# Optimization experiments

Hardware: AMD Instinct MI355X
Metric: run time of the kernel (lower is better)

## Reference

```python
import jax, jax.numpy as jnp
import numpy as np

N_PP = 8192      # number of papers (nodes_num_pp)
N_A = 8192       # number of authors
N_AP = N_PP + N_A  # nodes_num_ap (stacked paper+author id space)
DIM = 16
E = 262144
ALPHA = 0.5


def _cdist(x, y):
    # Euclidean cdist via Gram trick; avoids (B, A, D) broadcast intermediate.
    x2 = jnp.sum(x * x, axis=-1)[:, None]
    y2 = jnp.sum(y * y, axis=-1)[None, :]
    d2 = x2 + y2 - 2.0 * (x @ y.T)
    return jnp.sqrt(jnp.maximum(d2, 0.0))


def setup_inputs() -> dict:
    key = jax.random.key(0)
    ks = jax.random.split(key, 8)
    p_star = jax.random.normal(ks[0], (N_PP, DIM), dtype=jnp.float32)
    p = jax.random.normal(ks[1], (N_PP, DIM), dtype=jnp.float32)
    a = jax.random.normal(ks[2], (N_A, DIM), dtype=jnp.float32)
    beta_ap = 2.0 * jax.random.uniform(ks[3], (N_AP,), dtype=jnp.float32) - 1.0
    gamma_pp = 2.0 * jax.random.uniform(ks[4], (2 * N_PP,), dtype=jnp.float32) - 1.0
    edges_pp = jax.random.randint(ks[5], (2, E), 0, N_PP)
    e_ap0 = jax.random.randint(ks[6], (E,), 0, N_PP)
    e_ap1 = jax.random.randint(ks[7], (E,), N_PP, N_AP)
    edges_ap = jnp.stack([e_ap0, e_ap1])
    p_star_nodes = jnp.arange(N_PP, dtype=jnp.int32)
    p_nodes = jnp.arange(N_PP, dtype=jnp.int32)
    a_nodes = jnp.arange(N_A, dtype=jnp.int32) + N_PP
    return {"p_star": p_star, "p": p, "a": a, "beta_ap": beta_ap,
            "gamma_pp": gamma_pp, "edges_pp": edges_pp, "edges_ap": edges_ap,
            "p_star_nodes": p_star_nodes, "p_nodes": p_nodes, "a_nodes": a_nodes}


def reference(p_star, p, a, beta_ap, gamma_pp, edges_pp, edges_ap,
              p_star_nodes, p_nodes, a_nodes):
    # ---------- paper-paper (pp) term ----------
    ps_sel = p_star[p_star_nodes]                    # (B, D)
    p_sel = p[p_nodes]                               # (P, D)
    g_ps = gamma_pp[p_star_nodes]                    # (B,)
    g_p = gamma_pp[p_nodes + N_PP]                   # (P,)
    # gamma_mat.T - dist_mat, shape (B, P)
    m_pp = jnp.exp(g_ps[:, None] + g_p[None, :] - _cdist(ps_sel, p_sel))
    nonlink_pp = jnp.sum(jnp.triu(m_pp, k=1))        # strict upper triangle
    gamma_pair = gamma_pp[edges_pp[0]] + gamma_pp[edges_pp[1] + N_PP]
    d_pp = jnp.linalg.norm(p_star[edges_pp[0]] - p[edges_pp[1]], axis=-1)
    link_pp = jnp.sum(gamma_pair - d_pp)
    nll_pp = -(link_pp - nonlink_pp)

    # ---------- author-paper (ap) term ----------
    a_sel = a[a_nodes - N_PP]                        # (A, D)
    b_ps = beta_ap[p_star_nodes]                     # (B,)
    b_a = beta_ap[a_nodes]                           # (A,)
    # intended math: beta_mat.T - dist_mat, shape (B, A)
    m_ap = jnp.exp(b_ps[:, None] + b_a[None, :] - _cdist(ps_sel, a_sel))
    nonlink_ap = jnp.sum(m_ap)
    beta_pair = beta_ap[edges_ap[0]] + beta_ap[edges_ap[1]]
    d_ap = jnp.linalg.norm(p_star[edges_ap[0]] - a[edges_ap[1] - N_PP], axis=-1)
    link_ap = jnp.sum(beta_pair - d_ap)
    nll_ap = -(link_ap - nonlink_ap)

    n_p = p_nodes.shape[0]
    n_a = a_nodes.shape[0]
    return ALPHA * nll_pp / n_p + (1.0 - ALPHA) * nll_ap / n_a
```

## Files before the change

kernel.cpp:

```cpp
#include <hip/hip_runtime.h>
#include <stdint.h>

#define N_PP   8192
#define N_A    8192
#define DIM    16
#define NEDGE  262144
#define LOG2E  1.4426950408889634f
#define CH     32

#define WS_PSBF 64
#define WS_PBF  (WS_PSBF + 65536)
#define WS_ABF  (WS_PBF  + 65536)
#define WS_X2PS (WS_ABF  + 65536)
#define WS_Y2P  (WS_X2PS + 8192)
#define WS_Y2A  (WS_Y2P  + 8192)
#define WS_EGC  (WS_Y2A  + 8192)
#define WS_EBC  (WS_EGC  + 8192)
#define WS_GL2  (WS_EBC  + 8192)
#define WS_BL2  (WS_GL2  + 8192)

#define NB_AP  512
#define NB_PP  512
#define NB_EPP 256
#define NB_EAP 256
#define NB_TOTAL (NB_AP + NB_PP + NB_EPP + NB_EAP)

typedef short    bf16x8 __attribute__((ext_vector_type(8)));
typedef float    f32x4  __attribute__((ext_vector_type(4)));
typedef unsigned u32x4  __attribute__((ext_vector_type(4)));

__device__ __forceinline__ float waveReduce(float v) {
#pragma unroll
    for (int off = 32; off > 0; off >>= 1)
        v += __shfl_down(v, off, 64);
    return v;
}

__device__ __forceinline__ unsigned bf16_rne(float f) {
    unsigned u = __builtin_bit_cast(unsigned, f);
    return (u + 0x7FFFu + ((u >> 16) & 1u)) >> 16;
}
__device__ __forceinline__ unsigned packbf2(float a, float b) {
    return bf16_rne(a) | (bf16_rne(b) << 16);
}

__device__ __forceinline__ void gload_lds(const uint32_t* g, uint32_t* l) {
    __builtin_amdgcn_global_load_lds(
        (const __attribute__((address_space(1))) void*)(uintptr_t)g,
        (__attribute__((address_space(3))) void*)(unsigned)(uintptr_t)l,
        16, 0, 0);
}

__global__ __launch_bounds__(256) void precompute_kernel(
    const float* __restrict__ p_star, const float* __restrict__ p,
    const float* __restrict__ a, const float* __restrict__ beta_ap,
    const float* __restrict__ gamma_pp, float* __restrict__ ws)
{
    const int g = blockIdx.x * 256 + threadIdx.x;
    if (g < 8) ws[g] = 0.0f;

    if (g < 3 * 8192) {
        const int arr = g >> 13, idx = g & 8191;
        const float* src = arr == 0 ? p_star : (arr == 1 ? p : a);
        const int bfo = arr == 0 ? WS_PSBF : (arr == 1 ? WS_PBF : WS_ABF);
        const int n2o = arr == 0 ? WS_X2PS : (arr == 1 ? WS_Y2P : WS_Y2A);
        const float4* rp = (const float4*)(src + idx * DIM);
        float4 f0 = rp[0], f1 = rp[1], f2 = rp[2], f3 = rp[3];
        float n2 = f0.x*f0.x + f0.y*f0.y + f0.z*f0.z + f0.w*f0.w
                 + f1.x*f1.x + f1.y*f1.y + f1.z*f1.z + f1.w*f1.w
                 + f2.x*f2.x + f2.y*f2.y + f2.z*f2.z + f2.w*f2.w
                 + f3.x*f3.x + f3.y*f3.y + f3.z*f3.z + f3.w*f3.w;
        u32x4 u0 = { packbf2(f0.x, f0.y), packbf2(f0.z, f0.w),
                     packbf2(f1.x, f1.y), packbf2(f1.z, f1.w) };
        u32x4 u1 = { packbf2(f2.x, f2.y), packbf2(f2.z, f2.w),
                     packbf2(f3.x, f3.y), packbf2(f3.z, f3.w) };
        u32x4* dst = (u32x4*)(ws + bfo) + idx * 2;
        dst[0] = u0; dst[1] = u1;
        ws[n2o + idx] = n2;
    } else if (g < 7 * 8192) {
        const int h = g - 3 * 8192, q = h >> 13, i = h & 8191;
        if      (q == 0) ws[WS_EGC + i] = __expf(gamma_pp[8192 + i]);
        else if (q == 1) ws[WS_EBC + i] = __expf(beta_ap[8192 + i]);
        else if (q == 2) ws[WS_GL2 + i] = gamma_pp[i] * LOG2E;
        else             ws[WS_BL2 + i] = beta_ap[i] * LOG2E;
    }
}

__global__ void main_kernel(
    const float* __restrict__ p_star, const float* __restrict__ p,
    const float* __restrict__ a, const float* __restrict__ beta_ap,
    const float* __restrict__ gamma_pp, const int* __restrict__ edges_pp,
    const int* __restrict__ edges_ap, float* __restrict__ ws,
    float* __restrict__ out)
{
    __shared__ uint32_t sbuf[5120];
    __shared__ float smred[4];
    const int b = blockIdx.x, tid = threadIdx.x, wid = tid >> 6;
    const int lane = tid & 63, quad = lane >> 4, l16 = lane & 15;

    float val = 0.f;
    int slot;

    if (b < NB_AP + NB_PP) {
        const bool isPP = (b >= NB_AP);
        const int  bb   = isPP ? b - NB_AP : b;
        const int  g    = isPP ? 127 - (bb >> 2) : (bb >> 2);
        const int  q    = bb & 3;
        const int  s    = (g << 2) + wid;
        slot = isPP ? 0 : 2;

        const uint32_t* Xbf = (const uint32_t*)(ws + WS_PSBF);
        const uint32_t* Ybf = (const uint32_t*)(ws + (isPP ? WS_PBF : WS_ABF));
        const float* x2a = ws + WS_X2PS;
        const float* y2  = ws + (isPP ? WS_Y2P : WS_Y2A);
        const float* gl2 = ws + (isPP ? WS_GL2 : WS_BL2);
        const float* EcA = ws + (isPP ? WS_EGC : WS_EBC);

        const int j = (s << 4) + l16;
        u32x4 bu = {0u, 0u, 0u, 0u};
        if (quad < 2) bu = *(const u32x4*)(Ybf + j * 8 + (quad << 2));
        const bf16x8 bfrag = __builtin_bit_cast(bf16x8, bu);
        const float y2c = y2[j];
        const float Ec  = EcA[j];
        const f32x4 zero4 = {0.f, 0.f, 0.f, 0.f};

        const int len = isPP ? ((g << 2) + 4) : 512;
        const int nch = (len + CH - 1) / CH;
        const int c0 = (q * nch) >> 2, c1 = ((q + 1) * nch) >> 2;

        float acc = 0.f;
        for (int c = c0; c < c1; ++c) {
            const int t0 = c << 5;
            __syncthreads();
            for (int k = wid; k < 20; k += 4) {
                const uint32_t* gsrc;
                int loff;
                if (k < 16)      { gsrc = Xbf + (t0 << 7) + (k << 8);
                                   loff = k << 8; }
                else if (k < 18) { gsrc = (const uint32_t*)(x2a + (t0 << 4)) + ((k - 16) << 8);
                                   loff = 4096 + ((k - 16) << 8); }
                else             { gsrc = (const uint32_t*)(gl2 + (t0 << 4)) + ((k - 18) << 8);
                                   loff = 4608 + ((k - 18) << 8); }
                gload_lds(gsrc + (lane << 2), &sbuf[loff]);
            }
            __syncthreads();
            const int tF = isPP ? (s < t0 + CH ? s : t0 + CH) : t0 + CH;
            for (int t = t0; t < tF; ++t) {
                const int tl = t - t0;
                u32x4 au = {0u, 0u, 0u, 0u};
                if (quad < 2)
                    au = *(const u32x4*)&sbuf[(tl << 7) + (l16 << 3) + (quad << 2)];
                const f32x4 x24 = *(const f32x4*)((const float*)sbuf + 4096 + (tl << 4) + (quad << 2));
                const f32x4 ag4 = *(const f32x4*)((const float*)sbuf + 4608 + (tl << 4) + (quad << 2));
                f32x4 d = __builtin_amdgcn_mfma_f32_16x16x32_bf16(
                    __builtin_bit_cast(bf16x8, au), bfrag, zero4, 0, 0, 0);
#pragma unroll
                for (int r = 0; r < 4; ++r) {
                    float d2 = fmaf(-2.f, d[r], x24[r] + y2c);
                    d2 = fmaxf(d2, 0.f);
                    acc += __builtin_amdgcn_exp2f(
                        fmaf(-LOG2E, __builtin_amdgcn_sqrtf(d2), ag4[r]));
                }
            }
            if (isPP && s >= t0 && s < t0 + CH) {
                const int tl = s - t0;
                u32x4 au = {0u, 0u, 0u, 0u};
                if (quad < 2)
                    au = *(const u32x4*)&sbuf[(tl << 7) + (l16 << 3) + (quad << 2)];
                const f32x4 x24 = *(const f32x4*)((const float*)sbuf + 4096 + (tl << 4) + (quad << 2));
                const f32x4 ag4 = *(const f32x4*)((const float*)sbuf + 4608 + (tl << 4) + (quad << 2));
                f32x4 d = __builtin_amdgcn_mfma_f32_16x16x32_bf16(
                    __builtin_bit_cast(bf16x8, au), bfrag, zero4, 0, 0, 0);
#pragma unroll
                for (int r = 0; r < 4; ++r) {
                    float d2 = fmaf(-2.f, d[r], x24[r] + y2c);
                    d2 = fmaxf(d2, 0.f);
                    float term = __builtin_amdgcn_exp2f(
                        fmaf(-LOG2E, __builtin_amdgcn_sqrtf(d2), ag4[r]));
                    if (l16 <= (quad << 2) + r) term = 0.f;
                    acc += term;
                }
            }
        }
        val = acc * Ec;
    } else {
        const int  eb   = b - (NB_AP + NB_PP);
        const bool isPP = (eb < NB_EPP);
        const int  base = (isPP ? eb : eb - NB_EPP) * 256 + tid;
        slot = isPP ? 1 : 3;
        float sum = 0.f;
#pragma unroll
        for (int k = 0; k < 4; ++k) {
            const int e = base + k * 65536;
            const float* yrow;
            float bias;
            int e0;
            if (isPP) {
                e0 = edges_pp[e];
                int e1 = edges_pp[NEDGE + e];
                yrow = p + e1 * DIM;
                bias = gamma_pp[e0] + gamma_pp[N_PP + e1];
            } else {
                e0 = edges_ap[e];
                int e1 = edges_ap[NEDGE + e];
                yrow = a + (e1 - N_PP) * DIM;
                bias = beta_ap[e0] + beta_ap[e1];
            }
            const float4* xp = (const float4*)(p_star + e0 * DIM);
            const float4* yp = (const float4*)yrow;
            float d2 = 0.f;
#pragma unroll
            for (int kk = 0; kk < 4; ++kk) {
                float4 xv = xp[kk], yv = yp[kk];
                float dx = xv.x - yv.x, dy = xv.y - yv.y,
                      dz = xv.z - yv.z, dw = xv.w - yv.w;
                d2 += dx*dx + dy*dy + dz*dz + dw*dw;
            }
            sum += bias - __builtin_amdgcn_sqrtf(d2);
        }
        val = sum;
    }

    float wsum = waveReduce(val);
    if ((tid & 63) == 0) smred[wid] = wsum;
    __syncthreads();
    if (tid == 0) {
        atomicAdd(&ws[slot], smred[0] + smred[1] + smred[2] + smred[3]);
        __threadfence();
        unsigned old = atomicAdd((unsigned*)(ws + 4), 1u);
        if (old == NB_TOTAL - 1) {
            float s0 = atomicAdd(&ws[0], 0.f), s1 = atomicAdd(&ws[1], 0.f);
            float s2 = atomicAdd(&ws[2], 0.f), s3 = atomicAdd(&ws[3], 0.f);
            out[0] = 0.5f * (s0 - s1) / (float)N_PP
                   + 0.5f * (s2 - s3) / (float)N_A;
        }
    }
}

extern "C" void kernel_launch(void* const* d_in, const int* in_sizes, int n_in,
                              void* d_out, int out_size, void* d_ws, size_t ws_size,
                              hipStream_t stream) {
    const float* p_star   = (const float*)d_in[0];
    const float* p        = (const float*)d_in[1];
    const float* a        = (const float*)d_in[2];
    const float* beta_ap  = (const float*)d_in[3];
    const float* gamma_pp = (const float*)d_in[4];
    const int*   edges_pp = (const int*)d_in[5];
    const int*   edges_ap = (const int*)d_in[6];

    float* ws  = (float*)d_ws;
    float* out = (float*)d_out;

    hipLaunchKernelGGL(precompute_kernel, dim3(224), dim3(256), 0, stream,
                       p_star, p, a, beta_ap, gamma_pp, ws);
    hipLaunchKernelGGL(main_kernel, dim3(NB_TOTAL), dim3(256), 0, stream,
                       p_star, p, a, beta_ap, gamma_pp, edges_pp, edges_ap, ws, out);
}
```

Before: 146.0 us.

## Move edge sums into precompute kernel and retile pairwise blocks per chunk

```diff
diff --git a/kernel.cpp b/kernel.cpp
--- a/kernel.cpp
+++ b/kernel.cpp
@@ -2,28 +2,25 @@
 #include <stdint.h>
 
 #define N_PP   8192
-#define N_A    8192
 #define DIM    16
 #define NEDGE  262144
 #define LOG2E  1.4426950408889634f
-#define CH     32
-
-#define WS_PSBF 64
-#define WS_PBF  (WS_PSBF + 65536)
-#define WS_ABF  (WS_PBF  + 65536)
-#define WS_X2PS (WS_ABF  + 65536)
-#define WS_Y2P  (WS_X2PS + 8192)
-#define WS_Y2A  (WS_Y2P  + 8192)
-#define WS_EGC  (WS_Y2A  + 8192)
-#define WS_EBC  (WS_EGC  + 8192)
-#define WS_GL2  (WS_EBC  + 8192)
-#define WS_BL2  (WS_GL2  + 8192)
-
-#define NB_AP  512
-#define NB_PP  512
-#define NB_EPP 256
-#define NB_EAP 256
-#define NB_TOTAL (NB_AP + NB_PP + NB_EPP + NB_EAP)
+
+#define WS_EDGE  8
+#define WS_PSBF  512
+#define WS_PBF   (WS_PSBF + 65536)
+#define WS_ABF   (WS_PBF  + 65536)
+#define WS_X2PS  (WS_ABF  + 65536)
+#define WS_Y2P   (WS_X2PS + 8192)
+#define WS_Y2A   (WS_Y2P  + 8192)
+#define WS_EGC   (WS_Y2A  + 8192)
+#define WS_EBC   (WS_EGC  + 8192)
+#define WS_GL2   (WS_EBC  + 8192)
+#define WS_BL2   (WS_GL2  + 8192)
+
+#define NQ_AP  1024
+#define NQ_PP  544
+#define NB_MAT (NQ_AP + NQ_PP)
 
 typedef short    bf16x8 __attribute__((ext_vector_type(8)));
 typedef float    f32x4  __attribute__((ext_vector_type(4)));
@@ -51,147 +48,51 @@
         16, 0, 0);
 }
 
-__global__ __launch_bounds__(256) void precompute_kernel(
-    const float* __restrict__ p_star, const float* __restrict__ p,
-    const float* __restrict__ a, const float* __restrict__ beta_ap,
-    const float* __restrict__ gamma_pp, float* __restrict__ ws)
-{
-    const int g = blockIdx.x * 256 + threadIdx.x;
-    if (g < 8) ws[g] = 0.0f;
-
-    if (g < 3 * 8192) {
-        const int arr = g >> 13, idx = g & 8191;
-        const float* src = arr == 0 ? p_star : (arr == 1 ? p : a);
-        const int bfo = arr == 0 ? WS_PSBF : (arr == 1 ? WS_PBF : WS_ABF);
-        const int n2o = arr == 0 ? WS_X2PS : (arr == 1 ? WS_Y2P : WS_Y2A);
-        const float4* rp = (const float4*)(src + idx * DIM);
-        float4 f0 = rp[0], f1 = rp[1], f2 = rp[2], f3 = rp[3];
-        float n2 = f0.x*f0.x + f0.y*f0.y + f0.z*f0.z + f0.w*f0.w
-                 + f1.x*f1.x + f1.y*f1.y + f1.z*f1.z + f1.w*f1.w
-                 + f2.x*f2.x + f2.y*f2.y + f2.z*f2.z + f2.w*f2.w
-                 + f3.x*f3.x + f3.y*f3.y + f3.z*f3.z + f3.w*f3.w;
-        u32x4 u0 = { packbf2(f0.x, f0.y), packbf2(f0.z, f0.w),
-                     packbf2(f1.x, f1.y), packbf2(f1.z, f1.w) };
-        u32x4 u1 = { packbf2(f2.x, f2.y), packbf2(f2.z, f2.w),
-                     packbf2(f3.x, f3.y), packbf2(f3.z, f3.w) };
-        u32x4* dst = (u32x4*)(ws + bfo) + idx * 2;
-        dst[0] = u0; dst[1] = u1;
-        ws[n2o + idx] = n2;
-    } else if (g < 7 * 8192) {
-        const int h = g - 3 * 8192, q = h >> 13, i = h & 8191;
-        if      (q == 0) ws[WS_EGC + i] = __expf(gamma_pp[8192 + i]);
-        else if (q == 1) ws[WS_EBC + i] = __expf(beta_ap[8192 + i]);
-        else if (q == 2) ws[WS_GL2 + i] = gamma_pp[i] * LOG2E;
-        else             ws[WS_BL2 + i] = beta_ap[i] * LOG2E;
-    }
-}
-
-__global__ void main_kernel(
+__global__ __launch_bounds__(256) void pre_kernel(
     const float* __restrict__ p_star, const float* __restrict__ p,
     const float* __restrict__ a, const float* __restrict__ beta_ap,
     const float* __restrict__ gamma_pp, const int* __restrict__ edges_pp,
-    const int* __restrict__ edges_ap, float* __restrict__ ws,
-    float* __restrict__ out)
+    const int* __restrict__ edges_ap, float* __restrict__ ws)
 {
-    __shared__ uint32_t sbuf[5120];
-    __shared__ float smred[4];
-    const int b = blockIdx.x, tid = threadIdx.x, wid = tid >> 6;
-    const int lane = tid & 63, quad = lane >> 4, l16 = lane & 15;
-
-    float val = 0.f;
-    int slot;
-
-    if (b < NB_AP + NB_PP) {
-        const bool isPP = (b >= NB_AP);
-        const int  bb   = isPP ? b - NB_AP : b;
-        const int  g    = isPP ? 127 - (bb >> 2) : (bb >> 2);
-        const int  q    = bb & 3;
-        const int  s    = (g << 2) + wid;
-        slot = isPP ? 0 : 2;
-
-        const uint32_t* Xbf = (const uint32_t*)(ws + WS_PSBF);
-        const uint32_t* Ybf = (const uint32_t*)(ws + (isPP ? WS_PBF : WS_ABF));
-        const float* x2a = ws + WS_X2PS;
-        const float* y2  = ws + (isPP ? WS_Y2P : WS_Y2A);
-        const float* gl2 = ws + (isPP ? WS_GL2 : WS_BL2);
-        const float* EcA = ws + (isPP ? WS_EGC : WS_EBC);
-
-        const int j = (s << 4) + l16;
-        u32x4 bu = {0u, 0u, 0u, 0u};
-        if (quad < 2) bu = *(const u32x4*)(Ybf + j * 8 + (quad << 2));
-        const bf16x8 bfrag = __builtin_bit_cast(bf16x8, bu);
-        const float y2c = y2[j];
-        const float Ec  = EcA[j];
-        const f32x4 zero4 = {0.f, 0.f, 0.f, 0.f};
-
-        const int len = isPP ? ((g << 2) + 4) : 512;
-        const int nch = (len + CH - 1) / CH;
-        const int c0 = (q * nch) >> 2, c1 = ((q + 1) * nch) >> 2;
-
-        float acc = 0.f;
-        for (int c = c0; c < c1; ++c) {
-            const int t0 = c << 5;
-            __syncthreads();
-            for (int k = wid; k < 20; k += 4) {
-                const uint32_t* gsrc;
-                int loff;
-                if (k < 16)      { gsrc = Xbf + (t0 << 7) + (k << 8);
-                                   loff = k << 8; }
-                else if (k < 18) { gsrc = (const uint32_t*)(x2a + (t0 << 4)) + ((k - 16) << 8);
-                                   loff = 4096 + ((k - 16) << 8); }
-                else             { gsrc = (const uint32_t*)(gl2 + (t0 << 4)) + ((k - 18) << 8);
-                                   loff = 4608 + ((k - 18) << 8); }
-                gload_lds(gsrc + (lane << 2), &sbuf[loff]);
-            }
-            __syncthreads();
-            const int tF = isPP ? (s < t0 + CH ? s : t0 + CH) : t0 + CH;
-            for (int t = t0; t < tF; ++t) {
-                const int tl = t - t0;
-                u32x4 au = {0u, 0u, 0u, 0u};
-                if (quad < 2)
-                    au = *(const u32x4*)&sbuf[(tl << 7) + (l16 << 3) + (quad << 2)];
-                const f32x4 x24 = *(const f32x4*)((const float*)sbuf + 4096 + (tl << 4) + (quad << 2));
-                const f32x4 ag4 = *(const f32x4*)((const float*)sbuf + 4608 + (tl << 4) + (quad << 2));
-                f32x4 d = __builtin_amdgcn_mfma_f32_16x16x32_bf16(
-                    __builtin_bit_cast(bf16x8, au), bfrag, zero4, 0, 0, 0);
-#pragma unroll
-                for (int r = 0; r < 4; ++r) {
-                    float d2 = fmaf(-2.f, d[r], x24[r] + y2c);
-                    d2 = fmaxf(d2, 0.f);
-                    acc += __builtin_amdgcn_exp2f(
-                        fmaf(-LOG2E, __builtin_amdgcn_sqrtf(d2), ag4[r]));
-                }
-            }
-            if (isPP && s >= t0 && s < t0 + CH) {
-                const int tl = s - t0;
-                u32x4 au = {0u, 0u, 0u, 0u};
-                if (quad < 2)
-                    au = *(const u32x4*)&sbuf[(tl << 7) + (l16 << 3) + (quad << 2)];
-                const f32x4 x24 = *(const f32x4*)((const float*)sbuf + 4096 + (tl << 4) + (quad << 2));
-                const f32x4 ag4 = *(const f32x4*)((const float*)sbuf + 4608 + (tl << 4) + (quad << 2));
-                f32x4 d = __builtin_amdgcn_mfma_f32_16x16x32_bf16(
-                    __builtin_bit_cast(bf16x8, au), bfrag, zero4, 0, 0, 0);
-#pragma unroll
-                for (int r = 0; r < 4; ++r) {
-                    float d2 = fmaf(-2.f, d[r], x24[r] + y2c);
-                    d2 = fmaxf(d2, 0.f);
-                    float term = __builtin_amdgcn_exp2f(
-                        fmaf(-LOG2E, __builtin_amdgcn_sqrtf(d2), ag4[r]));
-                    if (l16 <= (quad << 2) + r) term = 0.f;
-                    acc += term;
-                }
-            }
-        }
-        val = acc * Ec;
+    const int b = blockIdx.x, tid = threadIdx.x;
+
+    if (b < 224) {
+        const int g = b * 256 + tid;
+        if (g < 8) ws[g] = 0.0f;
+        if (g < 3 * 8192) {
+            const int arr = g >> 13, idx = g & 8191;
+            const float* src = arr == 0 ? p_star : (arr == 1 ? p : a);
+            const int bfo = arr == 0 ? WS_PSBF : (arr == 1 ? WS_PBF : WS_ABF);
+            const int n2o = arr == 0 ? WS_X2PS : (arr == 1 ? WS_Y2P : WS_Y2A);
+            const float4* rp = (const float4*)(src + idx * DIM);
+            float4 f0 = rp[0], f1 = rp[1], f2 = rp[2], f3 = rp[3];
+            float n2 = f0.x*f0.x + f0.y*f0.y + f0.z*f0.z + f0.w*f0.w
+                     + f1.x*f1.x + f1.y*f1.y + f1.z*f1.z + f1.w*f1.w
+                     + f2.x*f2.x + f2.y*f2.y + f2.z*f2.z + f2.w*f2.w
+                     + f3.x*f3.x + f3.y*f3.y + f3.z*f3.z + f3.w*f3.w;
+            u32x4 u0 = { packbf2(f0.x, f0.y), packbf2(f0.z, f0.w),
+                         packbf2(f1.x, f1.y), packbf2(f1.z, f1.w) };
+            u32x4 u1 = { packbf2(f2.x, f2.y), packbf2(f2.z, f2.w),
+                         packbf2(f3.x, f3.y), packbf2(f3.z, f3.w) };
+            u32x4* dst = (u32x4*)(ws + bfo) + idx * 2;
+            dst[0] = u0; dst[1] = u1;
+            ws[n2o + idx] = n2;
+        } else if (g < 7 * 8192) {
+            const int h = g - 3 * 8192, q = h >> 13, i = h & 8191;
+            if      (q == 0) ws[WS_EGC + i] = __expf(gamma_pp[8192 + i]);
+            else if (q == 1) ws[WS_EBC + i] = __expf(beta_ap[8192 + i]);
+            else if (q == 2) ws[WS_GL2 + i] = gamma_pp[i] * LOG2E;
+            else             ws[WS_BL2 + i] = beta_ap[i] * LOG2E;
+        }
     } else {
-        const int  eb   = b - (NB_AP + NB_PP);
-        const bool isPP = (eb < NB_EPP);
-        const int  base = (isPP ? eb : eb - NB_EPP) * 256 + tid;
-        slot = isPP ? 1 : 3;
+        __shared__ float smred[4];
+        const int  eb   = b - 224;
+        const bool isPP = (eb < 128);
+        const int  base = (isPP ? eb : eb - 128) * 2048;
         float sum = 0.f;
 #pragma unroll
-        for (int k = 0; k < 4; ++k) {
-            const int e = base + k * 65536;
+        for (int k = 0; k < 8; ++k) {
+            const int e = base + k * 256 + tid;
             const float* yrow;
             float bias;
             int e0;
@@ -218,21 +119,122 @@
             }
             sum += bias - __builtin_amdgcn_sqrtf(d2);
         }
-        val = sum;
-    }
+        float wsum = waveReduce(sum);
+        if ((tid & 63) == 0) smred[tid >> 6] = wsum;
+        __syncthreads();
+        if (tid == 0)
+            ws[WS_EDGE + eb] = smred[0] + smred[1] + smred[2] + smred[3];
+    }
+}
+
+__global__ void main_kernel(float* __restrict__ ws, float* __restrict__ out)
+{
+    __shared__ uint32_t sbuf[5120];
+    __shared__ float smred[4];
+    const int b = blockIdx.x, tid = threadIdx.x, wid = tid >> 6;
+    const int lane = tid & 63, quad = lane >> 4, l16 = lane & 15;
+
+    const bool isPP = (b >= NQ_AP);
+    int g, c;
+    if (!isPP) { g = b >> 4; c = b & 15; }
+    else {
+        const int qq = b - NQ_AP;
+        int bnd = 0;
+        while (2 * (bnd + 1) * (bnd + 2) <= qq) ++bnd;
+        const int r = qq - 2 * bnd * (bnd + 1);
+        g = 4 * bnd + r / (bnd + 1);
+        c = r % (bnd + 1);
+    }
+    const int t0 = c << 5;
+
+    const uint32_t* Xbf = (const uint32_t*)(ws + WS_PSBF);
+    const uint32_t* Ybf = (const uint32_t*)(ws + (isPP ? WS_PBF : WS_ABF));
+    const float* x2a = ws + WS_X2PS;
+    const float* y2  = ws + (isPP ? WS_Y2P : WS_Y2A);
+    const float* gl2 = ws + (isPP ? WS_GL2 : WS_BL2);
+    const float* EcA = ws + (isPP ? WS_EGC : WS_EBC);
+
+    const int sA = (g << 3) + (wid << 1);
+    bf16x8 bfrag[2];
+    float  y2c[2], Ec[2];
+#pragma unroll
+    for (int ss = 0; ss < 2; ++ss) {
+        const int j = ((sA + ss) << 4) + l16;
+        u32x4 bu = {0u, 0u, 0u, 0u};
+        if (quad < 2) bu = *(const u32x4*)(Ybf + j * 8 + (quad << 2));
+        bfrag[ss] = __builtin_bit_cast(bf16x8, bu);
+        y2c[ss] = y2[j];
+        Ec[ss]  = EcA[j];
+    }
+
+    for (int k = wid; k < 20; k += 4) {
+        const uint32_t* gsrc;
+        int loff;
+        if (k < 16)      { gsrc = Xbf + (t0 << 7) + (k << 8);            loff = k << 8; }
+        else if (k < 18) { gsrc = (const uint32_t*)(x2a + (t0 << 4)) + ((k - 16) << 8);
+                           loff = 4096 + ((k - 16) << 8); }
+        else             { gsrc = (const uint32_t*)(gl2 + (t0 << 4)) + ((k - 18) << 8);
+                           loff = 4608 + ((k - 18) << 8); }
+        gload_lds(gsrc + (lane << 2), &sbuf[loff]);
+    }
+    __syncthreads();
+
+    const f32x4 zero4 = {0.f, 0.f, 0.f, 0.f};
+    float acc[2] = {0.f, 0.f};
+    const int tHi = isPP ? (sA + 1 < t0 + 32 ? sA + 2 : t0 + 32) : t0 + 32;
+    for (int t = t0; t < tHi; ++t) {
+        const int tl = t - t0;
+        const u32x4 au = *(const u32x4*)&sbuf[(tl << 7) + (l16 << 3) + ((quad & 1) << 2)];
+        const f32x4 x24 = *(const f32x4*)((const float*)sbuf + 4096 + (tl << 4) + (quad << 2));
+        const f32x4 ag4 = *(const f32x4*)((const float*)sbuf + 4608 + (tl << 4) + (quad << 2));
+#pragma unroll
+        for (int ss = 0; ss < 2; ++ss) {
+            const int s = sA + ss;
+            if (isPP && t > s) continue;
+            f32x4 d = __builtin_amdgcn_mfma_f32_16x16x32_bf16(
+                __builtin_bit_cast(bf16x8, au), bfrag[ss], zero4, 0, 0, 0);
+            if (!isPP || t < s) {
+#pragma unroll
+                for (int r = 0; r < 4; ++r) {
+                    float d2 = fmaf(-2.f, d[r], x24[r] + y2c[ss]);
+                    d2 = fmaxf(d2, 0.f);
+                    acc[ss] += __builtin_amdgcn_exp2f(
+                        fmaf(-LOG2E, __builtin_amdgcn_sqrtf(d2), ag4[r]));
+                }
+            } else {
+#pragma unroll
+                for (int r = 0; r < 4; ++r) {
+                    float d2 = fmaf(-2.f, d[r], x24[r] + y2c[ss]);
+                    d2 = fmaxf(d2, 0.f);
+                    float term = __builtin_amdgcn_exp2f(
+                        fmaf(-LOG2E, __builtin_amdgcn_sqrtf(d2), ag4[r]));
+                    if (l16 <= (quad << 2) + r) term = 0.f;
+                    acc[ss] += term;
+                }
+            }
+        }
+    }
+    const float val = acc[0] * Ec[0] + acc[1] * Ec[1];
 
     float wsum = waveReduce(val);
     if ((tid & 63) == 0) smred[wid] = wsum;
     __syncthreads();
     if (tid == 0) {
-        atomicAdd(&ws[slot], smred[0] + smred[1] + smred[2] + smred[3]);
+        atomicAdd(&ws[isPP ? 2 : 0], smred[0] + smred[1] + smred[2] + smred[3]);
         __threadfence();
         unsigned old = atomicAdd((unsigned*)(ws + 4), 1u);
-        if (old == NB_TOTAL - 1) {
-            float s0 = atomicAdd(&ws[0], 0.f), s1 = atomicAdd(&ws[1], 0.f);
-            float s2 = atomicAdd(&ws[2], 0.f), s3 = atomicAdd(&ws[3], 0.f);
-            out[0] = 0.5f * (s0 - s1) / (float)N_PP
-                   + 0.5f * (s2 - s3) / (float)N_A;
+        if (old == NB_MAT - 1) {
+            float s0 = atomicAdd(&ws[0], 0.f);
+            float s2 = atomicAdd(&ws[2], 0.f);
+            float lpp = 0.f, lap = 0.f;
+            for (int i = 0; i < 128; i += 4) {
+                const float4 v = *(const float4*)(ws + WS_EDGE + i);
+                const float4 u = *(const float4*)(ws + WS_EDGE + 128 + i);
+                lpp += v.x + v.y + v.z + v.w;
+                lap += u.x + u.y + u.z + u.w;
+            }
+            out[0] = 0.5f * (s0 - lpp) / (float)N_PP
+                   + 0.5f * (s2 - lap) / (float)N_PP;
         }
     }
 }
@@ -251,8 +253,7 @@
     float* ws  = (float*)d_ws;
     float* out = (float*)d_out;
 
-    hipLaunchKernelGGL(precompute_kernel, dim3(224), dim3(256), 0, stream,
-                       p_star, p, a, beta_ap, gamma_pp, ws);
-    hipLaunchKernelGGL(main_kernel, dim3(NB_TOTAL), dim3(256), 0, stream,
-                       p_star, p, a, beta_ap, gamma_pp, edges_pp, edges_ap, ws, out);
-}
+    hipLaunchKernelGGL(pre_kernel, dim3(480), dim3(256), 0, stream,
+                       p_star, p, a, beta_ap, gamma_pp, edges_pp, edges_ap, ws);
+    hipLaunchKernelGGL(main_kernel, dim3(NB_MAT), dim3(256), 0, stream, ws, out);
+}
```

Result: faster. 136.9 us (-6.2%).

## Fold squared norms into MFMA and retile pairwise blocks with two column tiles per wave

Applied to the files above, without the earlier changes.

```diff
diff --git a/kernel.cpp b/kernel.cpp
--- a/kernel.cpp
+++ b/kernel.cpp
@@ -2,28 +2,26 @@
 #include <stdint.h>
 
 #define N_PP   8192
-#define N_A    8192
 #define DIM    16
 #define NEDGE  262144
 #define LOG2E  1.4426950408889634f
-#define CH     32
-
-#define WS_PSBF 64
-#define WS_PBF  (WS_PSBF + 65536)
+#define CH     16
+
+#define WS_PSBF 512
+#define WS_PBF  (WS_PSBF + 98304)
 #define WS_ABF  (WS_PBF  + 65536)
-#define WS_X2PS (WS_ABF  + 65536)
-#define WS_Y2P  (WS_X2PS + 8192)
+#define WS_Y2P  (WS_ABF  + 65536)
 #define WS_Y2A  (WS_Y2P  + 8192)
 #define WS_EGC  (WS_Y2A  + 8192)
 #define WS_EBC  (WS_EGC  + 8192)
 #define WS_GL2  (WS_EBC  + 8192)
 #define WS_BL2  (WS_GL2  + 8192)
 
-#define NB_AP  512
-#define NB_PP  512
-#define NB_EPP 256
-#define NB_EAP 256
-#define NB_TOTAL (NB_AP + NB_PP + NB_EPP + NB_EAP)
+#define NQ_AP   2048
+#define NQ_PP   1056
+#define NB_MAT  (NQ_AP + NQ_PP)
+#define NB_EDGE 256
+#define NB_TOTAL (NB_MAT + NB_EDGE)
 
 typedef short    bf16x8 __attribute__((ext_vector_type(8)));
 typedef float    f32x4  __attribute__((ext_vector_type(4)));
@@ -51,7 +49,7 @@
         16, 0, 0);
 }
 
-__global__ __launch_bounds__(256) void precompute_kernel(
+__global__ __launch_bounds__(256) void pre_kernel(
     const float* __restrict__ p_star, const float* __restrict__ p,
     const float* __restrict__ a, const float* __restrict__ beta_ap,
     const float* __restrict__ gamma_pp, float* __restrict__ ws)
@@ -59,11 +57,25 @@
     const int g = blockIdx.x * 256 + threadIdx.x;
     if (g < 8) ws[g] = 0.0f;
 
-    if (g < 3 * 8192) {
-        const int arr = g >> 13, idx = g & 8191;
-        const float* src = arr == 0 ? p_star : (arr == 1 ? p : a);
-        const int bfo = arr == 0 ? WS_PSBF : (arr == 1 ? WS_PBF : WS_ABF);
-        const int n2o = arr == 0 ? WS_X2PS : (arr == 1 ? WS_Y2P : WS_Y2A);
+    if (g < 8192) {
+        const float4* rp = (const float4*)(p_star + g * DIM);
+        float4 f0 = rp[0], f1 = rp[1], f2 = rp[2], f3 = rp[3];
+        float x2 = f0.x*f0.x + f0.y*f0.y + f0.z*f0.z + f0.w*f0.w
+                 + f1.x*f1.x + f1.y*f1.y + f1.z*f1.z + f1.w*f1.w
+                 + f2.x*f2.x + f2.y*f2.y + f2.z*f2.z + f2.w*f2.w
+                 + f3.x*f3.x + f3.y*f3.y + f3.z*f3.z + f3.w*f3.w;
+        u32x4 u0 = { packbf2(-2.f*f0.x, -2.f*f0.y), packbf2(-2.f*f0.z, -2.f*f0.w),
+                     packbf2(-2.f*f1.x, -2.f*f1.y), packbf2(-2.f*f1.z, -2.f*f1.w) };
+        u32x4 u1 = { packbf2(-2.f*f2.x, -2.f*f2.y), packbf2(-2.f*f2.z, -2.f*f2.w),
+                     packbf2(-2.f*f3.x, -2.f*f3.y), packbf2(-2.f*f3.z, -2.f*f3.w) };
+        u32x4 u2 = { packbf2(x2, 1.0f), 0u, 0u, 0u };
+        uint32_t* dst = (uint32_t*)(ws + WS_PSBF) + g * 12;
+        *(u32x4*)dst = u0; *(u32x4*)(dst + 4) = u1; *(u32x4*)(dst + 8) = u2;
+    } else if (g < 3 * 8192) {
+        const int arr = (g >> 13) - 1, idx = g & 8191;
+        const float* src = arr == 0 ? p : a;
+        const int bfo = arr == 0 ? WS_PBF : WS_ABF;
+        const int n2o = arr == 0 ? WS_Y2P : WS_Y2A;
         const float4* rp = (const float4*)(src + idx * DIM);
         float4 f0 = rp[0], f1 = rp[1], f2 = rp[2], f3 = rp[3];
         float n2 = f0.x*f0.x + f0.y*f0.y + f0.z*f0.z + f0.w*f0.w
@@ -93,7 +105,7 @@
     const int* __restrict__ edges_ap, float* __restrict__ ws,
     float* __restrict__ out)
 {
-    __shared__ uint32_t sbuf[5120];
+    __shared__ uint32_t sbuf[3328];
     __shared__ float smred[4];
     const int b = blockIdx.x, tid = threadIdx.x, wid = tid >> 6;
     const int lane = tid & 63, quad = lane >> 4, l16 = lane & 15;
@@ -101,97 +113,122 @@
     float val = 0.f;
     int slot;
 
-    if (b < NB_AP + NB_PP) {
-        const bool isPP = (b >= NB_AP);
-        const int  bb   = isPP ? b - NB_AP : b;
-        const int  g    = isPP ? 127 - (bb >> 2) : (bb >> 2);
-        const int  q    = bb & 3;
-        const int  s    = (g << 2) + wid;
+    if (b < NB_MAT) {
+        const bool isPP = (b >= NQ_AP);
+        int g, c;
+        if (!isPP) { g = b >> 5; c = b & 31; }
+        else {
+            const int qq = b - NQ_AP;
+            int m = 0;
+            while ((m + 1) * (m + 2) <= qq) ++m;
+            const int r = qq - m * (m + 1);
+            const int dv = r / (m + 1);
+            g = 2 * m + dv; c = r - dv * (m + 1);
+        }
+        const int t0 = c << 4;
         slot = isPP ? 0 : 2;
 
         const uint32_t* Xbf = (const uint32_t*)(ws + WS_PSBF);
         const uint32_t* Ybf = (const uint32_t*)(ws + (isPP ? WS_PBF : WS_ABF));
-        const float* x2a = ws + WS_X2PS;
         const float* y2  = ws + (isPP ? WS_Y2P : WS_Y2A);
         const float* gl2 = ws + (isPP ? WS_GL2 : WS_BL2);
         const float* EcA = ws + (isPP ? WS_EGC : WS_EBC);
 
-        const int j = (s << 4) + l16;
-        u32x4 bu = {0u, 0u, 0u, 0u};
-        if (quad < 2) bu = *(const u32x4*)(Ybf + j * 8 + (quad << 2));
-        const bf16x8 bfrag = __builtin_bit_cast(bf16x8, bu);
-        const float y2c = y2[j];
-        const float Ec  = EcA[j];
+        const int sA = (g << 3) + (wid << 1);
+        bf16x8 bfrag[2];
+        float  Ec[2];
+#pragma unroll
+        for (int ss = 0; ss < 2; ++ss) {
+            const int j = ((sA + ss) << 4) + l16;
+            u32x4 bu = {0u, 0u, 0u, 0u};
+            if (quad < 2)       bu = *(const u32x4*)(Ybf + j * 8 + (quad << 2));
+            else if (quad == 2) bu.x = packbf2(1.0f, y2[j]);
+            bfrag[ss] = __builtin_bit_cast(bf16x8, bu);
+            Ec[ss] = EcA[j];
+        }
+
+        for (int k = wid; k < 13; k += 4) {
+            const uint32_t* gsrc;
+            int loff;
+            if (k < 12) { gsrc = Xbf + t0 * 192 + (k << 8); loff = k << 8; }
+            else        { gsrc = (const uint32_t*)(gl2 + (t0 << 4)); loff = 3072; }
+            gload_lds(gsrc + (lane << 2), &sbuf[loff]);
+        }
+        __syncthreads();
+
         const f32x4 zero4 = {0.f, 0.f, 0.f, 0.f};
-
-        const int len = isPP ? ((g << 2) + 4) : 512;
-        const int nch = (len + CH - 1) / CH;
-        const int c0 = (q * nch) >> 2, c1 = ((q + 1) * nch) >> 2;
-
-        float acc = 0.f;
-        for (int c = c0; c < c1; ++c) {
-            const int t0 = c << 5;
-            __syncthreads();
-            for (int k = wid; k < 20; k += 4) {
-                const uint32_t* gsrc;
-                int loff;
-                if (k < 16)      { gsrc = Xbf + (t0 << 7) + (k << 8);
-                                   loff = k << 8; }
-                else if (k < 18) { gsrc = (const uint32_t*)(x2a + (t0 << 4)) + ((k - 16) << 8);
-                                   loff = 4096 + ((k - 16) << 8); }
-                else             { gsrc = (const uint32_t*)(gl2 + (t0 << 4)) + ((k - 18) << 8);
-                                   loff = 4608 + ((k - 18) << 8); }
-                gload_lds(gsrc + (lane << 2), &sbuf[loff]);
-            }
-            __syncthreads();
-            const int tF = isPP ? (s < t0 + CH ? s : t0 + CH) : t0 + CH;
-            for (int t = t0; t < tF; ++t) {
-                const int tl = t - t0;
-                u32x4 au = {0u, 0u, 0u, 0u};
-                if (quad < 2)
-                    au = *(const u32x4*)&sbuf[(tl << 7) + (l16 << 3) + (quad << 2)];
-                const f32x4 x24 = *(const f32x4*)((const float*)sbuf + 4096 + (tl << 4) + (quad << 2));
-                const f32x4 ag4 = *(const f32x4*)((const float*)sbuf + 4608 + (tl << 4) + (quad << 2));
-                f32x4 d = __builtin_amdgcn_mfma_f32_16x16x32_bf16(
-                    __builtin_bit_cast(bf16x8, au), bfrag, zero4, 0, 0, 0);
+        const int aq4 = (quad < 2 ? quad : 2) << 2;
+        float acc0 = 0.f, acc1 = 0.f;
+
+        auto full_tile = [&](int t) {
+            const int tl = t - t0;
+            const u32x4 au = *(const u32x4*)&sbuf[tl * 192 + l16 * 12 + aq4];
+            const f32x4 ag4 = *(const f32x4*)((const float*)sbuf + 3072 + (tl << 4) + (quad << 2));
+            f32x4 d0 = __builtin_amdgcn_mfma_f32_16x16x32_bf16(
+                __builtin_bit_cast(bf16x8, au), bfrag[0], zero4, 0, 0, 0);
+            f32x4 d1 = __builtin_amdgcn_mfma_f32_16x16x32_bf16(
+                __builtin_bit_cast(bf16x8, au), bfrag[1], zero4, 0, 0, 0);
+#pragma unroll
+            for (int r = 0; r < 4; ++r) {
+                float q0 = fmaxf(d0[r], 0.f), q1 = fmaxf(d1[r], 0.f);
+                acc0 += __builtin_amdgcn_exp2f(
+                    fmaf(-LOG2E, __builtin_amdgcn_sqrtf(q0), ag4[r]));
+                acc1 += __builtin_amdgcn_exp2f(
+                    fmaf(-LOG2E, __builtin_amdgcn_sqrtf(q1), ag4[r]));
+            }
+        };
+
+        const int tFull = isPP ? (sA < t0 + CH ? sA : t0 + CH) : t0 + CH;
+        int t = t0;
+        for (; t + 1 < tFull; t += 2) { full_tile(t); full_tile(t + 1); }
+        if (t < tFull) full_tile(t);
+
+        if (isPP && sA < t0 + CH) {
+            {
+                const int tl = sA - t0;
+                const u32x4 au = *(const u32x4*)&sbuf[tl * 192 + l16 * 12 + aq4];
+                const f32x4 ag4 = *(const f32x4*)((const float*)sbuf + 3072 + (tl << 4) + (quad << 2));
+                f32x4 d0 = __builtin_amdgcn_mfma_f32_16x16x32_bf16(
+                    __builtin_bit_cast(bf16x8, au), bfrag[0], zero4, 0, 0, 0);
+                f32x4 d1 = __builtin_amdgcn_mfma_f32_16x16x32_bf16(
+                    __builtin_bit_cast(bf16x8, au), bfrag[1], zero4, 0, 0, 0);
 #pragma unroll
                 for (int r = 0; r < 4; ++r) {
-                    float d2 = fmaf(-2.f, d[r], x24[r] + y2c);
-                    d2 = fmaxf(d2, 0.f);
-                    acc += __builtin_amdgcn_exp2f(
-                        fmaf(-LOG2E, __builtin_amdgcn_sqrtf(d2), ag4[r]));
+                    float q0 = fmaxf(d0[r], 0.f), q1 = fmaxf(d1[r], 0.f);
+                    float t0v = __builtin_amdgcn_exp2f(
+                        fmaf(-LOG2E, __builtin_amdgcn_sqrtf(q0), ag4[r]));
+                    if (l16 <= (quad << 2) + r) t0v = 0.f;
+                    acc0 += t0v;
+                    acc1 += __builtin_amdgcn_exp2f(
+                        fmaf(-LOG2E, __builtin_amdgcn_sqrtf(q1), ag4[r]));
                 }
             }
-            if (isPP && s >= t0 && s < t0 + CH) {
-                const int tl = s - t0;
-                u32x4 au = {0u, 0u, 0u, 0u};
-                if (quad < 2)
-                    au = *(const u32x4*)&sbuf[(tl << 7) + (l16 << 3) + (quad << 2)];
-                const f32x4 x24 = *(const f32x4*)((const float*)sbuf + 4096 + (tl << 4) + (quad << 2));
-                const f32x4 ag4 = *(const f32x4*)((const float*)sbuf + 4608 + (tl << 4) + (quad << 2));
-                f32x4 d = __builtin_amdgcn_mfma_f32_16x16x32_bf16(
-                    __builtin_bit_cast(bf16x8, au), bfrag, zero4, 0, 0, 0);
+            {
+                const int tl = sA + 1 - t0;
+                const u32x4 au = *(const u32x4*)&sbuf[tl * 192 + l16 * 12 + aq4];
+                const f32x4 ag4 = *(const f32x4*)((const float*)sbuf + 3072 + (tl << 4) + (quad << 2));
+                f32x4 d1 = __builtin_amdgcn_mfma_f32_16x16x32_bf16(
+                    __builtin_bit_cast(bf16x8, au), bfrag[1], zero4, 0, 0, 0);
 #pragma unroll
                 for (int r = 0; r < 4; ++r) {
-                    float d2 = fmaf(-2.f, d[r], x24[r] + y2c);
-                    d2 = fmaxf(d2, 0.f);
-                    float term = __builtin_amdgcn_exp2f(
-                        fmaf(-LOG2E, __builtin_amdgcn_sqrtf(d2), ag4[r]));
-                    if (l16 <= (quad << 2) + r) term = 0.f;
-                    acc += term;
+                    float q1 = fmaxf(d1[r], 0.f);
+                    float t1v = __builtin_amdgcn_exp2f(
+                        fmaf(-LOG2E, __builtin_amdgcn_sqrtf(q1), ag4[r]));
+                    if (l16 <= (quad << 2) + r) t1v = 0.f;
+                    acc1 += t1v;
                 }
             }
         }
-        val = acc * Ec;
+        val = acc0 * Ec[0] + acc1 * Ec[1];
     } else {
-        const int  eb   = b - (NB_AP + NB_PP);
-        const bool isPP = (eb < NB_EPP);
-        const int  base = (isPP ? eb : eb - NB_EPP) * 256 + tid;
+        const int  eb   = b - NB_MAT;
+        const bool isPP = (eb < 128);
+        const int  base = (isPP ? eb : eb - 128) * 2048;
         slot = isPP ? 1 : 3;
         float sum = 0.f;
 #pragma unroll
-        for (int k = 0; k < 4; ++k) {
-            const int e = base + k * 65536;
+        for (int k = 0; k < 8; ++k) {
+            const int e = base + k * 256 + tid;
             const float* yrow;
             float bias;
             int e0;
@@ -232,7 +269,7 @@
             float s0 = atomicAdd(&ws[0], 0.f), s1 = atomicAdd(&ws[1], 0.f);
             float s2 = atomicAdd(&ws[2], 0.f), s3 = atomicAdd(&ws[3], 0.f);
             out[0] = 0.5f * (s0 - s1) / (float)N_PP
-                   + 0.5f * (s2 - s3) / (float)N_A;
+                   + 0.5f * (s2 - s3) / (float)N_PP;
         }
     }
 }
@@ -251,7 +288,7 @@
     float* ws  = (float*)d_ws;
     float* out = (float*)d_out;
 
-    hipLaunchKernelGGL(precompute_kernel, dim3(224), dim3(256), 0, stream,
+    hipLaunchKernelGGL(pre_kernel, dim3(224), dim3(256), 0, stream,
                        p_star, p, a, beta_ap, gamma_pp, ws);
     hipLaunchKernelGGL(main_kernel, dim3(NB_TOTAL), dim3(256), 0, stream,
                        p_star, p, a, beta_ap, gamma_pp, edges_pp, edges_ap, ws, out);
```

Measured after the change: 209.6 us. 43.5% more time.
